# Kernel tuning notes

Hardware: AMD Instinct MI355X
Metric: run time of the kernel (lower is better)

## Reference

```python
import jax, jax.numpy as jnp
import numpy as np

N_ROIS = 2000
FH, FW, C = 50, 50, 512
PH, PW = 7, 7
N_CLASS = 21
IMG = 800
FC_IN = PH * PW * C  # 25088
FC_OUT = 4096


def crop_and_resize(img, boxes, ph, pw):
    """Faithful jax port of tf.image.crop_and_resize (bilinear, extrapolation 0).
    img: [H, W, C]; boxes: [N, 4] normalized (y1, x1, y2, x2). Returns [N, ph, pw, C]."""
    H, W, _ = img.shape
    y1, x1, y2, x2 = boxes[:, 0], boxes[:, 1], boxes[:, 2], boxes[:, 3]
    iy = jnp.arange(ph, dtype=boxes.dtype)
    ix = jnp.arange(pw, dtype=boxes.dtype)
    # TF sampling grid: in_y = y1*(H-1) + i * (y2-y1)*(H-1)/(crop_h-1)
    in_y = y1[:, None] * (H - 1) + iy[None, :] * ((y2 - y1)[:, None] * (H - 1) / (ph - 1))  # [N, ph]
    in_x = x1[:, None] * (W - 1) + ix[None, :] * ((x2 - x1)[:, None] * (W - 1) / (pw - 1))  # [N, pw]
    y0f = jnp.floor(in_y); x0f = jnp.floor(in_x)
    ylerp = (in_y - y0f)[:, :, None, None]   # [N, ph, 1, 1]
    xlerp = (in_x - x0f)[:, None, :, None]   # [N, 1, pw, 1]
    y0 = jnp.clip(y0f, 0, H - 1).astype(jnp.int32)
    y1i = jnp.clip(y0f + 1, 0, H - 1).astype(jnp.int32)
    x0 = jnp.clip(x0f, 0, W - 1).astype(jnp.int32)
    x1i = jnp.clip(x0f + 1, 0, W - 1).astype(jnp.int32)

    def gather(yi, xi):  # [N,ph],[N,pw] -> [N,ph,pw,C]
        return img[yi[:, :, None], xi[:, None, :]]

    top = gather(y0, x0) * (1 - xlerp) + gather(y0, x1i) * xlerp
    bot = gather(y1i, x0) * (1 - xlerp) + gather(y1i, x1i) * xlerp
    out = top * (1 - ylerp) + bot * ylerp
    valid = ((in_y >= 0) & (in_y <= H - 1))[:, :, None] & ((in_x >= 0) & (in_x <= W - 1))[:, None, :]
    return jnp.where(valid[..., None], out, jnp.zeros((), out.dtype))


def setup_inputs() -> dict:
    key = jax.random.key(0)
    kf, ky, kx, k1, k2, k3, k4, k5, k6 = jax.random.split(key, 9)
    feature = jax.random.normal(kf, (1, FH, FW, C), dtype=jnp.float32)
    # valid boxes in original-image coordinates: y1<y2, x1<x2 within [0, IMG]
    ys = jnp.sort(jax.random.uniform(ky, (N_ROIS, 2), dtype=jnp.float32) * IMG, axis=1)
    xs = jnp.sort(jax.random.uniform(kx, (N_ROIS, 2), dtype=jnp.float32) * IMG, axis=1)
    rois = jnp.stack([ys[:, 0], xs[:, 0], ys[:, 1], xs[:, 1]], axis=1)
    W_fc = jax.random.normal(k1, (FC_IN, FC_OUT), dtype=jnp.float32) * 0.01
    b_fc = jnp.zeros((FC_OUT,), dtype=jnp.float32)
    W_loc = jax.random.normal(k3, (FC_OUT, N_CLASS * 4), dtype=jnp.float32) * 0.01
    b_loc = jnp.zeros((N_CLASS * 4,), dtype=jnp.float32)
    W_score = jax.random.normal(k5, (FC_OUT, N_CLASS), dtype=jnp.float32) * 0.01
    b_score = jnp.zeros((N_CLASS,), dtype=jnp.float32)
    return {"feature": feature, "rois": rois, "img_h": IMG, "img_w": IMG,
            "W_fc": W_fc, "b_fc": b_fc, "W_loc": W_loc, "b_loc": b_loc,
            "W_score": W_score, "b_score": b_score}


def reference(feature, rois, img_h, img_w, W_fc, b_fc, W_loc, b_loc, W_score, b_score):
    norm = jnp.array([img_h, img_w, img_h, img_w], dtype=jnp.float32)
    boxes = rois / norm                      # normalized [y1,x1,y2,x2]
    pool = crop_and_resize(feature[0], boxes, PH, PW)  # [N, 7, 7, 512]
    flat = pool.reshape(rois.shape[0], -1)   # [N, 25088]
    fc = flat @ W_fc + b_fc                  # [N, 4096]
    roi_cls_locs = fc @ W_loc + b_loc        # [N, 84]
    roi_scores = fc @ W_score + b_score      # [N, 21]
    return roi_cls_locs, roi_scores
```

## Files before the change

### kernel.cpp

```cpp
#include <hip/hip_runtime.h>
#include <stdint.h>


typedef float          f32x4 __attribute__((ext_vector_type(4)));
typedef __bf16         bfx8  __attribute__((ext_vector_type(8)));
typedef unsigned short u16x8 __attribute__((ext_vector_type(8)));

#define KBIG 25088
#define NMID 4096
#define NROIS 2000

__device__ __forceinline__ unsigned short f2bf(float f) {
  unsigned int u = __float_as_uint(f);
  unsigned int r = (u + 0x7fffu + ((u >> 16) & 1u)) >> 16;
  return (unsigned short)r;
}

__device__ __forceinline__ void gll16(const void* g, void* l) {
  __builtin_amdgcn_global_load_lds(
      (const __attribute__((address_space(1))) void*)(uintptr_t)(g),
      (__attribute__((address_space(3))) void*)(uintptr_t)(l), 16, 0, 0);
}

__global__ __launch_bounds__(256) void k_wcat(const float* __restrict__ Wl,
                                              const float* __restrict__ Ws,
                                              unsigned short* __restrict__ WcatT) {
  int idx = blockIdx.x * 256 + threadIdx.x;
  int c = idx >> 12;
  int k = idx & 4095;
  float v = 0.0f;
  if (c < 84)       v = Wl[k * 84 + c];
  else if (c < 105) v = Ws[k * 21 + (c - 84)];
  WcatT[idx] = f2bf(v);
}

__global__ __launch_bounds__(256) void k_bc(const float* __restrict__ bfc,
                                            const float* __restrict__ Wl,
                                            const float* __restrict__ Ws,
                                            const float* __restrict__ bl,
                                            const float* __restrict__ bs,
                                            float* __restrict__ bc) {
  int c = blockIdx.x;
  int t = threadIdx.x;
  __shared__ float red[256];
  float p = 0.0f;
  if (c < 105) {
    for (int k = t; k < 4096; k += 256) {
      float w = (c < 84) ? Wl[k * 84 + c] : Ws[k * 21 + (c - 84)];
      p += bfc[k] * w;
    }
  }
  red[t] = p;
  __syncthreads();
  for (int s = 128; s > 0; s >>= 1) {
    if (t < s) red[t] += red[t + s];
    __syncthreads();
  }
  if (t == 0) {
    float bias = (c < 84) ? bl[c] : (c < 105 ? bs[c - 84] : 0.0f);
    bc[c] = (c < 105) ? (red[0] + bias) : 0.0f;
  }
}

__global__ __launch_bounds__(256) void k_pool(const float* __restrict__ F,
                                              const float* __restrict__ rois,
                                              const int* __restrict__ ihp,
                                              const int* __restrict__ iwp,
                                              unsigned short* __restrict__ A) {
  const int r = blockIdx.x;
  const int t = threadIdx.x;
  const float ih = (float)ihp[0], iw = (float)iwp[0];
  const float y1 = rois[r * 4 + 0] / ih;
  const float x1 = rois[r * 4 + 1] / iw;
  const float y2 = rois[r * 4 + 2] / ih;
  const float x2 = rois[r * 4 + 3] / iw;
  const float sy = (y2 - y1) * 49.0f / 6.0f;
  const float sx = (x2 - x1) * 49.0f / 6.0f;
  const int ch = t * 2;
  unsigned int* __restrict__ Arow = (unsigned int*)(A + (size_t)r * KBIG);
  for (int cell = 0; cell < 49; ++cell) {
    const int iy = cell / 7, ix = cell - iy * 7;
    const float in_y = y1 * 49.0f + (float)iy * sy;
    const float in_x = x1 * 49.0f + (float)ix * sx;
    const float y0f = floorf(in_y), x0f = floorf(in_x);
    const float yl = in_y - y0f, xl = in_x - x0f;
    const int y0  = (int)fminf(fmaxf(y0f, 0.0f), 49.0f);
    const int y1i = (int)fminf(fmaxf(y0f + 1.0f, 0.0f), 49.0f);
    const int x0  = (int)fminf(fmaxf(x0f, 0.0f), 49.0f);
    const int x1i = (int)fminf(fmaxf(x0f + 1.0f, 0.0f), 49.0f);
    const bool valid = (in_y >= 0.0f) && (in_y <= 49.0f) &&
                       (in_x >= 0.0f) && (in_x <= 49.0f);
    float2 f00 = *(const float2*)&F[(y0 * 50 + x0) * 512 + ch];
    float2 f01 = *(const float2*)&F[(y0 * 50 + x1i) * 512 + ch];
    float2 f10 = *(const float2*)&F[(y1i * 50 + x0) * 512 + ch];
    float2 f11 = *(const float2*)&F[(y1i * 50 + x1i) * 512 + ch];
    float o0 = 0.0f, o1 = 0.0f;
    if (valid) {
      float t0 = f00.x * (1.0f - xl) + f01.x * xl;
      float t1 = f00.y * (1.0f - xl) + f01.y * xl;
      float b0 = f10.x * (1.0f - xl) + f11.x * xl;
      float b1 = f10.y * (1.0f - xl) + f11.y * xl;
      o0 = t0 * (1.0f - yl) + b0 * yl;
      o1 = t1 * (1.0f - yl) + b1 * yl;
    }
    unsigned int pk = (unsigned int)f2bf(o0) | ((unsigned int)f2bf(o1) << 16);
    Arow[(cell * 512 + ch) >> 1] = pk;
  }
}


__global__ __launch_bounds__(256) void k_gemm1(const float* __restrict__ Wfc,
                                               const unsigned short* __restrict__ WcatT,
                                               unsigned short* __restrict__ WcT) {
  __shared__ __align__(16) char sA[8192];
  __shared__ __align__(16) char sB[16384];
  const int t = threadIdx.x;
  const int lane = t & 63, wid = t >> 6;
  const int wm = wid >> 1, wn = wid & 1;
  const int l15 = lane & 15, l4 = lane >> 4;
  const int mtile = blockIdx.x * 64;
  const int jlog = (t & 7) ^ ((t >> 3) & 7);
  f32x4 acc[2][4] = {};

  const int arow = t >> 2;
  const int akq  = t & 3;
  const float* aptr = Wfc + (size_t)(mtile + arow) * NMID + akq * 16;
  char* awr0 = sA + arow * 128 + ((((akq << 1) + 0) ^ (arow & 7)) << 4);
  char* awr1 = sA + arow * 128 + ((((akq << 1) + 1) ^ (arow & 7)) << 4);

  for (int ks = 0; ks < 64; ++ks) {
    const int k0 = ks * 64;
    f32x4 v0 = *(const f32x4*)(aptr + k0 + 0);
    f32x4 v1 = *(const f32x4*)(aptr + k0 + 4);
    f32x4 v2 = *(const f32x4*)(aptr + k0 + 8);
    f32x4 v3 = *(const f32x4*)(aptr + k0 + 12);
#pragma unroll
    for (int c = 0; c < 4; ++c) {
      const int row = c * 32 + (t >> 3);
      gll16(WcatT + (size_t)row * NMID + k0 + jlog * 8, sB + c * 4096 + wid * 1024);
    }
    u16x8 p0, p1;
#pragma unroll
    for (int i = 0; i < 4; ++i) {
      p0[i]     = f2bf(v0[i]);
      p0[i + 4] = f2bf(v1[i]);
      p1[i]     = f2bf(v2[i]);
      p1[i + 4] = f2bf(v3[i]);
    }
    *(u16x8*)awr0 = p0;
    *(u16x8*)awr1 = p1;
    __syncthreads();
#pragma unroll
    for (int kh = 0; kh < 2; ++kh) {
      bfx8 af[2], bfr[4];
#pragma unroll
      for (int mi = 0; mi < 2; ++mi) {
        const int row = wm * 32 + mi * 16 + l15;
        af[mi] = *(const bfx8*)(sA + row * 128 + ((((kh << 2) + l4) ^ (row & 7)) << 4));
      }
#pragma unroll
      for (int ni = 0; ni < 4; ++ni) {
        const int row = wn * 64 + ni * 16 + l15;
        bfr[ni] = *(const bfx8*)(sB + row * 128 + ((((kh << 2) + l4) ^ (row & 7)) << 4));
      }
#pragma unroll
      for (int mi = 0; mi < 2; ++mi)
#pragma unroll
        for (int ni = 0; ni < 4; ++ni)
          acc[mi][ni] = __builtin_amdgcn_mfma_f32_16x16x32_bf16(af[mi], bfr[ni], acc[mi][ni], 0, 0, 0);
    }
    __syncthreads();
  }
#pragma unroll
  for (int mi = 0; mi < 2; ++mi)
#pragma unroll
    for (int ni = 0; ni < 4; ++ni)
#pragma unroll
      for (int i = 0; i < 4; ++i) {
        const int gm = mtile + wm * 32 + mi * 16 + l4 * 4 + i;
        const int gn = wn * 64 + ni * 16 + l15;
        WcT[(size_t)gn * KBIG + gm] = f2bf(acc[mi][ni][i]);
      }
}

__global__ __launch_bounds__(256) void k_gemm2(const unsigned short* __restrict__ Ap,
                                               const unsigned short* __restrict__ WcT,
                                               float* __restrict__ P) {
  __shared__ __align__(16) char sA[8192];
  __shared__ __align__(16) char sB[16384];
  const int t = threadIdx.x;
  const int lane = t & 63, wid = t >> 6;
  const int wm = wid >> 1, wn = wid & 1;
  const int l15 = lane & 15, l4 = lane >> 4;
  const int bid = blockIdx.x;
  const int mt = bid >> 3, sp = bid & 7;
  const int kbase = sp * 3136;
  const int jlog = (t & 7) ^ ((t >> 3) & 7);
  f32x4 acc[2][4] = {};

  int ar0 = mt * 64 + (t >> 3);
  int ar1 = ar0 + 32;
  if (ar0 > NROIS - 1) ar0 = NROIS - 1;
  if (ar1 > NROIS - 1) ar1 = NROIS - 1;
  const unsigned short* asrc0 = Ap + (size_t)ar0 * KBIG + jlog * 8;
  const unsigned short* asrc1 = Ap + (size_t)ar1 * KBIG + jlog * 8;

  for (int ks = 0; ks < 49; ++ks) {
    const int k0 = kbase + ks * 64;
    gll16(asrc0 + k0, sA + wid * 1024);
    gll16(asrc1 + k0, sA + 4096 + wid * 1024);
#pragma unroll
    for (int c = 0; c < 4; ++c) {
      const int row = c * 32 + (t >> 3);
      gll16(WcT + (size_t)row * KBIG + k0 + jlog * 8, sB + c * 4096 + wid * 1024);
    }
    __syncthreads();
#pragma unroll
    for (int kh = 0; kh < 2; ++kh) {
      bfx8 af[2], bfr[4];
#pragma unroll
      for (int mi = 0; mi < 2; ++mi) {
        const int row = wm * 32 + mi * 16 + l15;
        af[mi] = *(const bfx8*)(sA + row * 128 + ((((kh << 2) + l4) ^ (row & 7)) << 4));
      }
#pragma unroll
      for (int ni = 0; ni < 4; ++ni) {
        const int row = wn * 64 + ni * 16 + l15;
        bfr[ni] = *(const bfx8*)(sB + row * 128 + ((((kh << 2) + l4) ^ (row & 7)) << 4));
      }
#pragma unroll
      for (int mi = 0; mi < 2; ++mi)
#pragma unroll
        for (int ni = 0; ni < 4; ++ni)
          acc[mi][ni] = __builtin_amdgcn_mfma_f32_16x16x32_bf16(af[mi], bfr[ni], acc[mi][ni], 0, 0, 0);
    }
    __syncthreads();
  }
  float* out = P + (size_t)bid * 8192;
#pragma unroll
  for (int mi = 0; mi < 2; ++mi)
#pragma unroll
    for (int ni = 0; ni < 4; ++ni)
#pragma unroll
      for (int i = 0; i < 4; ++i)
        out[(wm * 32 + mi * 16 + l4 * 4 + i) * 128 + wn * 64 + ni * 16 + l15] = acc[mi][ni][i];
}

__global__ __launch_bounds__(128) void k_reduce(const float* __restrict__ P,
                                                const float* __restrict__ bc,
                                                float* __restrict__ out) {
  const int m = blockIdx.x;
  const int c = threadIdx.x;
  if (c >= 105) return;
  const int mt = m >> 6, r = m & 63;
  float sum = 0.0f;
#pragma unroll
  for (int s = 0; s < 8; ++s)
    sum += P[(size_t)((mt * 8 + s) * 8192) + r * 128 + c];
  sum += bc[c];
  if (c < 84) out[m * 84 + c] = sum;
  else        out[168000 + m * 21 + (c - 84)] = sum;
}

extern "C" void kernel_launch(void* const* d_in, const int* in_sizes, int n_in,
                              void* d_out, int out_size, void* d_ws, size_t ws_size,
                              hipStream_t stream) {
  const float* F    = (const float*)d_in[0];
  const float* rois = (const float*)d_in[1];
  const int*   ih   = (const int*)d_in[2];
  const int*   iw   = (const int*)d_in[3];
  const float* Wfc  = (const float*)d_in[4];
  const float* bfc  = (const float*)d_in[5];
  const float* Wl   = (const float*)d_in[6];
  const float* bl   = (const float*)d_in[7];
  const float* Ws   = (const float*)d_in[8];
  const float* bs   = (const float*)d_in[9];
  (void)in_sizes; (void)n_in; (void)out_size; (void)ws_size;

  char* ws = (char*)d_ws;
  unsigned short* Apool = (unsigned short*)(ws);
  unsigned short* WcatT = (unsigned short*)(ws + 100352000);
  unsigned short* WcT   = (unsigned short*)(ws + 101400576);
  float*          bc    = (float*)(ws + 107823104);
  float*          P     = (float*)(ws + 107823616);
  float*          out   = (float*)d_out;

  k_wcat  <<<2048, 256, 0, stream>>>(Wl, Ws, WcatT);
  k_bc    <<<128,  256, 0, stream>>>(bfc, Wl, Ws, bl, bs, bc);
  k_pool  <<<2000, 256, 0, stream>>>(F, rois, ih, iw, Apool);
  k_gemm1 <<<392,  256, 0, stream>>>(Wfc, WcatT, WcT);
  k_gemm2 <<<256,  256, 0, stream>>>(Apool, WcT, P);
  k_reduce<<<2000, 128, 0, stream>>>(P, bc, out);
}
```

Baseline: 257.7 us.

## Merge prep and pool/gemm1 launches, shrink gemm1 tiles, raise gemm2 split-K

Merges the weight-concat and bias kernels into one launch, and runs ROI pooling and the weight-fold GEMM as disjoint block ranges of a single launch. gemm1 tiles shrink from 64 to 32 rows, prefetch the next fp32 Wfc chunk during compute, and write packed 4-wide outputs. gemm2 split-K rises from 8 to 28 on a 2D grid, and the reduce sums 28 partials. The aim is fewer launches and more blocks to fill the CUs, paid for with a larger partial buffer and more reduction traffic.

```diff
diff --git a/kernel.cpp b/kernel.cpp
--- a/kernel.cpp
+++ b/kernel.cpp
@@ -5,15 +5,17 @@
 typedef float          f32x4 __attribute__((ext_vector_type(4)));
 typedef __bf16         bfx8  __attribute__((ext_vector_type(8)));
 typedef unsigned short u16x8 __attribute__((ext_vector_type(8)));
+typedef unsigned short u16x4 __attribute__((ext_vector_type(4)));
 
 #define KBIG 25088
 #define NMID 4096
 #define NROIS 2000
+#define G1BLOCKS 784
+#define SPLITS 28
 
 __device__ __forceinline__ unsigned short f2bf(float f) {
   unsigned int u = __float_as_uint(f);
-  unsigned int r = (u + 0x7fffu + ((u >> 16) & 1u)) >> 16;
-  return (unsigned short)r;
+  return (unsigned short)((u + 0x7fffu + ((u >> 16) & 1u)) >> 16);
 }
 
 __device__ __forceinline__ void gll16(const void* g, void* l) {
@@ -22,165 +24,153 @@
       (__attribute__((address_space(3))) void*)(uintptr_t)(l), 16, 0, 0);
 }
 
-__global__ __launch_bounds__(256) void k_wcat(const float* __restrict__ Wl,
+__global__ __launch_bounds__(256) void k_prep(const float* __restrict__ Wl,
                                               const float* __restrict__ Ws,
-                                              unsigned short* __restrict__ WcatT) {
-  int idx = blockIdx.x * 256 + threadIdx.x;
-  int c = idx >> 12;
-  int k = idx & 4095;
-  float v = 0.0f;
-  if (c < 84)       v = Wl[k * 84 + c];
-  else if (c < 105) v = Ws[k * 21 + (c - 84)];
-  WcatT[idx] = f2bf(v);
-}
-
-__global__ __launch_bounds__(256) void k_bc(const float* __restrict__ bfc,
-                                            const float* __restrict__ Wl,
-                                            const float* __restrict__ Ws,
-                                            const float* __restrict__ bl,
-                                            const float* __restrict__ bs,
-                                            float* __restrict__ bc) {
-  int c = blockIdx.x;
-  int t = threadIdx.x;
-  __shared__ float red[256];
-  float p = 0.0f;
-  if (c < 105) {
-    for (int k = t; k < 4096; k += 256) {
-      float w = (c < 84) ? Wl[k * 84 + c] : Ws[k * 21 + (c - 84)];
-      p += bfc[k] * w;
+                                              const float* __restrict__ bfc,
+                                              const float* __restrict__ bl,
+                                              const float* __restrict__ bs,
+                                              unsigned short* __restrict__ WcatT,
+                                              float* __restrict__ bc) {
+  if (blockIdx.x < 2048) {
+    int idx = blockIdx.x * 256 + threadIdx.x;
+    int c = idx >> 12, k = idx & 4095;
+    float v = 0.0f;
+    if (c < 84)       v = Wl[k * 84 + c];
+    else if (c < 105) v = Ws[k * 21 + (c - 84)];
+    WcatT[idx] = f2bf(v);
+  } else {
+    int c = blockIdx.x - 2048;
+    int t = threadIdx.x;
+    __shared__ float red[256];
+    float p = 0.0f;
+    if (c < 105) {
+      for (int k = t; k < 4096; k += 256) {
+        float w = (c < 84) ? Wl[k * 84 + c] : Ws[k * 21 + (c - 84)];
+        p += bfc[k] * w;
+      }
+    }
+    red[t] = p;
+    __syncthreads();
+    for (int s = 128; s > 0; s >>= 1) {
+      if (t < s) red[t] += red[t + s];
+      __syncthreads();
+    }
+    if (t == 0) {
+      float bias = (c < 84) ? bl[c] : (c < 105 ? bs[c - 84] : 0.0f);
+      bc[c] = (c < 105) ? (red[0] + bias) : 0.0f;
     }
   }
-  red[t] = p;
-  __syncthreads();
-  for (int s = 128; s > 0; s >>= 1) {
-    if (t < s) red[t] += red[t + s];
-    __syncthreads();
+}
+
+__global__ __launch_bounds__(256) void k_pool_gemm1(
+    const float* __restrict__ F, const float* __restrict__ rois,
+    const int* __restrict__ ihp, const int* __restrict__ iwp,
+    unsigned short* __restrict__ A,
+    const float* __restrict__ Wfc, const unsigned short* __restrict__ WcatT,
+    unsigned short* __restrict__ WcT) {
+  const int t = threadIdx.x;
+  if (blockIdx.x < G1BLOCKS) {
+    __shared__ __align__(16) char sA[4096];
+    __shared__ __align__(16) char sB[16384];
+    const int lane = t & 63, wid = t >> 6;
+    const int l15 = lane & 15, l4 = lane >> 4;
+    const int mtile = blockIdx.x * 32;
+    const int jlog = (t & 7) ^ ((t >> 3) & 7);
+    f32x4 acc[2][2] = {};
+
+    const int arow = t >> 3;
+    const int aj = t & 7;
+    const float* aptr = Wfc + (size_t)(mtile + arow) * NMID + aj * 8;
+    char* awr = sA + arow * 128 + ((aj ^ (arow & 7)) << 4);
+
+    f32x4 v0 = *(const f32x4*)(aptr);
+    f32x4 v1 = *(const f32x4*)(aptr + 4);
+    for (int ks = 0; ks < 64; ++ks) {
+      u16x8 p;
+#pragma unroll
+      for (int i = 0; i < 4; ++i) { p[i] = f2bf(v0[i]); p[i + 4] = f2bf(v1[i]); }
+      *(u16x8*)awr = p;
+#pragma unroll
+      for (int c = 0; c < 4; ++c)
+        gll16(WcatT + (size_t)(c * 32 + (t >> 3)) * NMID + ks * 64 + jlog * 8,
+              sB + c * 4096 + wid * 1024);
+      __syncthreads();
+      if (ks < 63) {
+        v0 = *(const f32x4*)(aptr + (ks + 1) * 64);
+        v1 = *(const f32x4*)(aptr + (ks + 1) * 64 + 4);
+      }
+#pragma unroll
+      for (int kh = 0; kh < 2; ++kh) {
+        bfx8 af[2], bfr[2];
+#pragma unroll
+        for (int mi = 0; mi < 2; ++mi) {
+          const int row = mi * 16 + l15;
+          af[mi] = *(const bfx8*)(sA + row * 128 + ((((kh << 2) + l4) ^ (row & 7)) << 4));
+        }
+#pragma unroll
+        for (int ni = 0; ni < 2; ++ni) {
+          const int row = wid * 32 + ni * 16 + l15;
+          bfr[ni] = *(const bfx8*)(sB + row * 128 + ((((kh << 2) + l4) ^ (row & 7)) << 4));
+        }
+#pragma unroll
+        for (int mi = 0; mi < 2; ++mi)
+#pragma unroll
+          for (int ni = 0; ni < 2; ++ni)
+            acc[mi][ni] = __builtin_amdgcn_mfma_f32_16x16x32_bf16(af[mi], bfr[ni], acc[mi][ni], 0, 0, 0);
+      }
+      __syncthreads();
+    }
+#pragma unroll
+    for (int mi = 0; mi < 2; ++mi)
+#pragma unroll
+      for (int ni = 0; ni < 2; ++ni) {
+        const int gm0 = mtile + mi * 16 + l4 * 4;
+        const int gn = wid * 32 + ni * 16 + l15;
+        u16x4 pk;
+#pragma unroll
+        for (int i = 0; i < 4; ++i) pk[i] = f2bf(acc[mi][ni][i]);
+        *(u16x4*)(WcT + (size_t)gn * KBIG + gm0) = pk;
+      }
+  } else {
+    const int r = blockIdx.x - G1BLOCKS;
+    const float ih = (float)ihp[0], iw = (float)iwp[0];
+    const float y1 = rois[r * 4 + 0] / ih;
+    const float x1 = rois[r * 4 + 1] / iw;
+    const float y2 = rois[r * 4 + 2] / ih;
+    const float x2 = rois[r * 4 + 3] / iw;
+    const float sy = (y2 - y1) * 49.0f / 6.0f;
+    const float sx = (x2 - x1) * 49.0f / 6.0f;
+    const int ch = t * 2;
+    unsigned int* __restrict__ Arow = (unsigned int*)(A + (size_t)r * KBIG);
+    for (int cell = 0; cell < 49; ++cell) {
+      const int iy = cell / 7, ix = cell - iy * 7;
+      const float in_y = y1 * 49.0f + (float)iy * sy;
+      const float in_x = x1 * 49.0f + (float)ix * sx;
+      const float y0f = floorf(in_y), x0f = floorf(in_x);
+      const float yl = in_y - y0f, xl = in_x - x0f;
+      const int y0  = (int)fminf(fmaxf(y0f, 0.0f), 49.0f);
+      const int y1i = (int)fminf(fmaxf(y0f + 1.0f, 0.0f), 49.0f);
+      const int x0  = (int)fminf(fmaxf(x0f, 0.0f), 49.0f);
+      const int x1i = (int)fminf(fmaxf(x0f + 1.0f, 0.0f), 49.0f);
+      const bool valid = (in_y >= 0.0f) && (in_y <= 49.0f) &&
+                         (in_x >= 0.0f) && (in_x <= 49.0f);
+      float2 f00 = *(const float2*)&F[(y0 * 50 + x0) * 512 + ch];
+      float2 f01 = *(const float2*)&F[(y0 * 50 + x1i) * 512 + ch];
+      float2 f10 = *(const float2*)&F[(y1i * 50 + x0) * 512 + ch];
+      float2 f11 = *(const float2*)&F[(y1i * 50 + x1i) * 512 + ch];
+      float o0 = 0.0f, o1 = 0.0f;
+      if (valid) {
+        float t0 = f00.x * (1.0f - xl) + f01.x * xl;
+        float t1 = f00.y * (1.0f - xl) + f01.y * xl;
+        float b0 = f10.x * (1.0f - xl) + f11.x * xl;
+        float b1 = f10.y * (1.0f - xl) + f11.y * xl;
+        o0 = t0 * (1.0f - yl) + b0 * yl;
+        o1 = t1 * (1.0f - yl) + b1 * yl;
+      }
+      Arow[(cell * 512 + ch) >> 1] =
+          (unsigned int)f2bf(o0) | ((unsigned int)f2bf(o1) << 16);
+    }
   }
-  if (t == 0) {
-    float bias = (c < 84) ? bl[c] : (c < 105 ? bs[c - 84] : 0.0f);
-    bc[c] = (c < 105) ? (red[0] + bias) : 0.0f;
-  }
-}
-
-__global__ __launch_bounds__(256) void k_pool(const float* __restrict__ F,
-                                              const float* __restrict__ rois,
-                                              const int* __restrict__ ihp,
-                                              const int* __restrict__ iwp,
-                                              unsigned short* __restrict__ A) {
-  const int r = blockIdx.x;
-  const int t = threadIdx.x;
-  const float ih = (float)ihp[0], iw = (float)iwp[0];
-  const float y1 = rois[r * 4 + 0] / ih;
-  const float x1 = rois[r * 4 + 1] / iw;
-  const float y2 = rois[r * 4 + 2] / ih;
-  const float x2 = rois[r * 4 + 3] / iw;
-  const float sy = (y2 - y1) * 49.0f / 6.0f;
-  const float sx = (x2 - x1) * 49.0f / 6.0f;
-  const int ch = t * 2;
-  unsigned int* __restrict__ Arow = (unsigned int*)(A + (size_t)r * KBIG);
-  for (int cell = 0; cell < 49; ++cell) {
-    const int iy = cell / 7, ix = cell - iy * 7;
-    const float in_y = y1 * 49.0f + (float)iy * sy;
-    const float in_x = x1 * 49.0f + (float)ix * sx;
-    const float y0f = floorf(in_y), x0f = floorf(in_x);
-    const float yl = in_y - y0f, xl = in_x - x0f;
-    const int y0  = (int)fminf(fmaxf(y0f, 0.0f), 49.0f);
-    const int y1i = (int)fminf(fmaxf(y0f + 1.0f, 0.0f), 49.0f);
-    const int x0  = (int)fminf(fmaxf(x0f, 0.0f), 49.0f);
-    const int x1i = (int)fminf(fmaxf(x0f + 1.0f, 0.0f), 49.0f);
-    const bool valid = (in_y >= 0.0f) && (in_y <= 49.0f) &&
-                       (in_x >= 0.0f) && (in_x <= 49.0f);
-    float2 f00 = *(const float2*)&F[(y0 * 50 + x0) * 512 + ch];
-    float2 f01 = *(const float2*)&F[(y0 * 50 + x1i) * 512 + ch];
-    float2 f10 = *(const float2*)&F[(y1i * 50 + x0) * 512 + ch];
-    float2 f11 = *(const float2*)&F[(y1i * 50 + x1i) * 512 + ch];
-    float o0 = 0.0f, o1 = 0.0f;
-    if (valid) {
-      float t0 = f00.x * (1.0f - xl) + f01.x * xl;
-      float t1 = f00.y * (1.0f - xl) + f01.y * xl;
-      float b0 = f10.x * (1.0f - xl) + f11.x * xl;
-      float b1 = f10.y * (1.0f - xl) + f11.y * xl;
-      o0 = t0 * (1.0f - yl) + b0 * yl;
-      o1 = t1 * (1.0f - yl) + b1 * yl;
-    }
-    unsigned int pk = (unsigned int)f2bf(o0) | ((unsigned int)f2bf(o1) << 16);
-    Arow[(cell * 512 + ch) >> 1] = pk;
-  }
-}
-
-
-__global__ __launch_bounds__(256) void k_gemm1(const float* __restrict__ Wfc,
-                                               const unsigned short* __restrict__ WcatT,
-                                               unsigned short* __restrict__ WcT) {
-  __shared__ __align__(16) char sA[8192];
-  __shared__ __align__(16) char sB[16384];
-  const int t = threadIdx.x;
-  const int lane = t & 63, wid = t >> 6;
-  const int wm = wid >> 1, wn = wid & 1;
-  const int l15 = lane & 15, l4 = lane >> 4;
-  const int mtile = blockIdx.x * 64;
-  const int jlog = (t & 7) ^ ((t >> 3) & 7);
-  f32x4 acc[2][4] = {};
-
-  const int arow = t >> 2;
-  const int akq  = t & 3;
-  const float* aptr = Wfc + (size_t)(mtile + arow) * NMID + akq * 16;
-  char* awr0 = sA + arow * 128 + ((((akq << 1) + 0) ^ (arow & 7)) << 4);
-  char* awr1 = sA + arow * 128 + ((((akq << 1) + 1) ^ (arow & 7)) << 4);
-
-  for (int ks = 0; ks < 64; ++ks) {
-    const int k0 = ks * 64;
-    f32x4 v0 = *(const f32x4*)(aptr + k0 + 0);
-    f32x4 v1 = *(const f32x4*)(aptr + k0 + 4);
-    f32x4 v2 = *(const f32x4*)(aptr + k0 + 8);
-    f32x4 v3 = *(const f32x4*)(aptr + k0 + 12);
-#pragma unroll
-    for (int c = 0; c < 4; ++c) {
-      const int row = c * 32 + (t >> 3);
-      gll16(WcatT + (size_t)row * NMID + k0 + jlog * 8, sB + c * 4096 + wid * 1024);
-    }
-    u16x8 p0, p1;
-#pragma unroll
-    for (int i = 0; i < 4; ++i) {
-      p0[i]     = f2bf(v0[i]);
-      p0[i + 4] = f2bf(v1[i]);
-      p1[i]     = f2bf(v2[i]);
-      p1[i + 4] = f2bf(v3[i]);
-    }
-    *(u16x8*)awr0 = p0;
-    *(u16x8*)awr1 = p1;
-    __syncthreads();
-#pragma unroll
-    for (int kh = 0; kh < 2; ++kh) {
-      bfx8 af[2], bfr[4];
-#pragma unroll
-      for (int mi = 0; mi < 2; ++mi) {
-        const int row = wm * 32 + mi * 16 + l15;
-        af[mi] = *(const bfx8*)(sA + row * 128 + ((((kh << 2) + l4) ^ (row & 7)) << 4));
-      }
-#pragma unroll
-      for (int ni = 0; ni < 4; ++ni) {
-        const int row = wn * 64 + ni * 16 + l15;
-        bfr[ni] = *(const bfx8*)(sB + row * 128 + ((((kh << 2) + l4) ^ (row & 7)) << 4));
-      }
-#pragma unroll
-      for (int mi = 0; mi < 2; ++mi)
-#pragma unroll
-        for (int ni = 0; ni < 4; ++ni)
-          acc[mi][ni] = __builtin_amdgcn_mfma_f32_16x16x32_bf16(af[mi], bfr[ni], acc[mi][ni], 0, 0, 0);
-    }
-    __syncthreads();
-  }
-#pragma unroll
-  for (int mi = 0; mi < 2; ++mi)
-#pragma unroll
-    for (int ni = 0; ni < 4; ++ni)
-#pragma unroll
-      for (int i = 0; i < 4; ++i) {
-        const int gm = mtile + wm * 32 + mi * 16 + l4 * 4 + i;
-        const int gn = wn * 64 + ni * 16 + l15;
-        WcT[(size_t)gn * KBIG + gm] = f2bf(acc[mi][ni][i]);
-      }
 }
 
 __global__ __launch_bounds__(256) void k_gemm2(const unsigned short* __restrict__ Ap,
@@ -192,9 +182,8 @@
   const int lane = t & 63, wid = t >> 6;
   const int wm = wid >> 1, wn = wid & 1;
   const int l15 = lane & 15, l4 = lane >> 4;
-  const int bid = blockIdx.x;
-  const int mt = bid >> 3, sp = bid & 7;
-  const int kbase = sp * 3136;
+  const int mt = blockIdx.x, sp = blockIdx.y;
+  const int kbase = sp * 896;
   const int jlog = (t & 7) ^ ((t >> 3) & 7);
   f32x4 acc[2][4] = {};
 
@@ -205,15 +194,14 @@
   const unsigned short* asrc0 = Ap + (size_t)ar0 * KBIG + jlog * 8;
   const unsigned short* asrc1 = Ap + (size_t)ar1 * KBIG + jlog * 8;
 
-  for (int ks = 0; ks < 49; ++ks) {
+  for (int ks = 0; ks < 14; ++ks) {
     const int k0 = kbase + ks * 64;
     gll16(asrc0 + k0, sA + wid * 1024);
     gll16(asrc1 + k0, sA + 4096 + wid * 1024);
 #pragma unroll
-    for (int c = 0; c < 4; ++c) {
-      const int row = c * 32 + (t >> 3);
-      gll16(WcT + (size_t)row * KBIG + k0 + jlog * 8, sB + c * 4096 + wid * 1024);
-    }
+    for (int c = 0; c < 4; ++c)
+      gll16(WcT + (size_t)(c * 32 + (t >> 3)) * KBIG + k0 + jlog * 8,
+            sB + c * 4096 + wid * 1024);
     __syncthreads();
 #pragma unroll
     for (int kh = 0; kh < 2; ++kh) {
@@ -236,7 +224,7 @@
     }
     __syncthreads();
   }
-  float* out = P + (size_t)bid * 8192;
+  float* out = P + (size_t)(mt * SPLITS + sp) * 8192;
 #pragma unroll
   for (int mi = 0; mi < 2; ++mi)
 #pragma unroll
@@ -255,8 +243,8 @@
   const int mt = m >> 6, r = m & 63;
   float sum = 0.0f;
 #pragma unroll
-  for (int s = 0; s < 8; ++s)
-    sum += P[(size_t)((mt * 8 + s) * 8192) + r * 128 + c];
+  for (int s = 0; s < SPLITS; ++s)
+    sum += P[(size_t)(mt * SPLITS + s) * 8192 + r * 128 + c];
   sum += bc[c];
   if (c < 84) out[m * 84 + c] = sum;
   else        out[168000 + m * 21 + (c - 84)] = sum;
@@ -285,10 +273,9 @@
   float*          P     = (float*)(ws + 107823616);
   float*          out   = (float*)d_out;
 
-  k_wcat  <<<2048, 256, 0, stream>>>(Wl, Ws, WcatT);
-  k_bc    <<<128,  256, 0, stream>>>(bfc, Wl, Ws, bl, bs, bc);
-  k_pool  <<<2000, 256, 0, stream>>>(F, rois, ih, iw, Apool);
-  k_gemm1 <<<392,  256, 0, stream>>>(Wfc, WcatT, WcT);
-  k_gemm2 <<<256,  256, 0, stream>>>(Apool, WcT, P);
-  k_reduce<<<2000, 128, 0, stream>>>(P, bc, out);
-}
+  k_prep      <<<2176, 256, 0, stream>>>(Wl, Ws, bfc, bl, bs, WcatT, bc);
+  k_pool_gemm1<<<G1BLOCKS + NROIS, 256, 0, stream>>>(F, rois, ih, iw, Apool,
+                                                     Wfc, WcatT, WcT);
+  k_gemm2     <<<dim3(32, SPLITS), 256, 0, stream>>>(Apool, WcT, P);
+  k_reduce    <<<NROIS, 128, 0, stream>>>(P, bc, out);
+}
```

After: 235.7 us. 1.09x faster.
